# Kernel optimization log

Hardware: AMD Instinct MI355X
Metric: run time of the kernel (lower is better)

## Reference

```python
import jax, jax.numpy as jnp
import numpy as np

N_NODES = 50000
N_EDGES = 800000
NODE_DIM = 64
EDGE_DIM = 16
HIDDEN = 128
EPS = 1e-5


def _linear_init(key, fan_in, fan_out):
    k1, k2 = jax.random.split(key)
    bound = 1.0 / np.sqrt(fan_in)
    W = jax.random.uniform(k1, (fan_in, fan_out), minval=-bound, maxval=bound, dtype=jnp.float32)
    b = jax.random.uniform(k2, (fan_out,), minval=-bound, maxval=bound, dtype=jnp.float32)
    return W, b


def batchnorm(h, gamma, beta):
    # BatchNorm1d in training mode: batch mean/var (biased), eps=1e-5
    mu = jnp.mean(h, axis=0, keepdims=True)
    var = jnp.mean((h - mu) ** 2, axis=0, keepdims=True)
    return (h - mu) * jax.lax.rsqrt(var + EPS) * gamma + beta


def setup_inputs() -> dict:
    key = jax.random.key(0)
    ks = jax.random.split(key, 8)
    x = jax.random.normal(ks[0], (N_NODES, NODE_DIM), dtype=jnp.float32)
    edge_index = jax.random.randint(ks[1], (2, N_EDGES), 0, N_NODES, dtype=jnp.int64)
    edge_attr = jax.random.normal(ks[2], (N_EDGES, EDGE_DIM), dtype=jnp.float32)
    We1, be1 = _linear_init(ks[3], 2 * NODE_DIM + EDGE_DIM, HIDDEN)
    We2, be2 = _linear_init(ks[4], HIDDEN, HIDDEN)
    Wm, bm = _linear_init(ks[5], HIDDEN, HIDDEN)
    Wn1, bn1 = _linear_init(ks[6], NODE_DIM + HIDDEN, HIDDEN)
    Wn2, bn2 = _linear_init(ks[7], HIDDEN, HIDDEN)
    ones = jnp.ones((HIDDEN,), jnp.float32)
    zeros = jnp.zeros((HIDDEN,), jnp.float32)
    return dict(x=x, edge_index=edge_index, edge_attr=edge_attr,
                We1=We1, be1=be1, ge=ones, bbe=zeros, We2=We2, be2=be2,
                Wm=Wm, bm=bm,
                Wn1=Wn1, bn1=bn1, gn=ones, bbn=zeros, Wn2=Wn2, bn2=bn2)


def reference(x, edge_index, edge_attr, We1, be1, ge, bbe, We2, be2, Wm, bm, Wn1, bn1, gn, bbn, Wn2, bn2):
    row, col = edge_index[0], edge_index[1]
    # gather + concat -> edge network (Linear, BN, ReLU, Linear)
    edge_input = jnp.concatenate([x[row], x[col], edge_attr], axis=-1)  # [E, 2n+e]
    h = jax.nn.relu(batchnorm(edge_input @ We1 + be1, ge, bbe))
    edge_features = h @ We2 + be2
    # message MLP (Linear, ReLU)
    messages = jax.nn.relu(edge_features @ Wm + bm)  # [E, H]
    # scatter-add into source nodes
    agg = jax.ops.segment_sum(messages, row, num_segments=N_NODES)  # [N, H]
    # node network (Linear, BN, ReLU, Linear)
    node_input = jnp.concatenate([x, agg], axis=-1)
    hn = jax.nn.relu(batchnorm(node_input @ Wn1 + bn1, gn, bbn))
    return hn @ Wn2 + bn2
```

## Files before the change

### kernel.cpp

```cpp
#include <hip/hip_runtime.h>
#include <stdint.h>

#define NNODES 50000
#define NEDGES 800000
#define H 128
#define BN_EPS 1e-5f

typedef short short8 __attribute__((ext_vector_type(8)));
typedef float f32x4 __attribute__((ext_vector_type(4)));

__device__ __forceinline__ float bf2f(unsigned short u) {
    unsigned int v = ((unsigned int)u) << 16;
    return __uint_as_float(v);
}
__device__ __forceinline__ unsigned short f2bf(float f) {
    unsigned int x = __float_as_uint(f);
    return (unsigned short)((x + 0x7FFFu + ((x >> 16) & 1u)) >> 16);
}
__device__ __forceinline__ short8 s8z() { short8 z = {0,0,0,0,0,0,0,0}; return z; }

template<int KB>
__device__ __forceinline__ void gemm_tile(const short* __restrict__ sA, const int SK,
                                          const unsigned short* __restrict__ WT, const int RK,
                                          const int n0, f32x4 acc[4][4], const int lane) {
    const int mr = lane & 15, quad = lane >> 4;
    const short* W = (const short*)WT;
    #pragma unroll
    for (int kb = 0; kb < KB; ++kb) {
        short8 a[4];
        #pragma unroll
        for (int mt = 0; mt < 4; ++mt)
            a[mt] = *(const short8*)&sA[(mt*16 + mr)*SK + kb*32 + quad*8];
        #pragma unroll
        for (int nt = 0; nt < 4; ++nt) {
            short8 b = *(const short8*)&W[(size_t)(n0 + nt*16 + mr)*RK + kb*32 + quad*8];
            #pragma unroll
            for (int mt = 0; mt < 4; ++mt)
                acc[mt][nt] = __builtin_amdgcn_mfma_f32_16x16x32_bf16(a[mt], b, acc[mt][nt], 0, 0, 0);
        }
    }
}

__global__ void k_fold(const float* __restrict__ We2, const float* __restrict__ be2,
                       const float* __restrict__ Wm, const float* __restrict__ bm,
                       float* __restrict__ W2m, float* __restrict__ b2m) {
    int j = threadIdx.x;
    int i = blockIdx.x;
    if (i < H) {
        float acc = 0.f;
        for (int k = 0; k < H; ++k) acc = fmaf(We2[i*H + k], Wm[k*H + j], acc);
        W2m[i*H + j] = acc;
    } else {
        float acc = bm[j];
        for (int k = 0; k < H; ++k) acc = fmaf(be2[k], Wm[k*H + j], acc);
        b2m[j] = acc;
    }
}

__global__ void k_prep2(const float* __restrict__ We1, const float* __restrict__ Wn1,
                        const float* __restrict__ Wn2, const float* __restrict__ W2m,
                        unsigned short* __restrict__ WabT, unsigned short* __restrict__ Wn1T,
                        unsigned short* __restrict__ Wn2T, unsigned short* __restrict__ W2mT,
                        unsigned short* __restrict__ WcT) {
    int i = blockIdx.x*256 + threadIdx.x;
    if (i < 16384) {
        int n = i >> 6, k = i & 63;
        WabT[n*64 + k] = f2bf(We1[(n < 128 ? k : 64 + k)*H + (n & 127)]);
    } else if (i < 40960) {
        int j = i - 16384; int n = j / 192, k = j - n*192;
        Wn1T[n*192 + k] = f2bf(Wn1[k*H + n]);
    } else if (i < 57344) {
        int j = i - 40960; int n = j >> 7, k = j & 127;
        Wn2T[n*H + k] = f2bf(Wn2[k*H + n]);
    } else if (i < 73728) {
        int j = i - 57344; int n = j >> 7, k = j & 127;
        W2mT[n*H + k] = f2bf(W2m[k*H + n]);
    } else if (i < 77824) {
        int j = i - 73728; int n = j >> 5, k = j & 31;
        WcT[n*32 + k] = (k < 16) ? f2bf(We1[(128 + k)*H + n]) : (unsigned short)0;
    }
}

__global__ void k_count(const int* __restrict__ ei, int* __restrict__ cnt) {
    int e = blockIdx.x*256 + threadIdx.x;
    if (e < NEDGES) atomicAdd(&cnt[ei[e]], 1);
}

__global__ void k_scan(const int* __restrict__ cnt, int* __restrict__ offsets,
                       int* __restrict__ cursor) {
    __shared__ int wsum[16];
    __shared__ int carry;
    const int tid = threadIdx.x;
    const int lane = tid & 63, wid = tid >> 6;
    if (tid == 0) carry = 0;
    for (int base = 0; base < NNODES; base += 1024) {
        int i = base + tid;
        int v = (i < NNODES) ? cnt[i] : 0;
        int xv = v;
        #pragma unroll
        for (int off = 1; off < 64; off <<= 1) {
            int y = __shfl_up(xv, off);
            if (lane >= off) xv += y;
        }
        if (lane == 63) wsum[wid] = xv;
        __syncthreads();
        if (tid == 0) {
            int a = carry;
            #pragma unroll
            for (int j = 0; j < 16; ++j) { int t = wsum[j]; wsum[j] = a; a += t; }
            carry = a;
        }
        __syncthreads();
        int excl = wsum[wid] + xv - v;
        if (i < NNODES) { offsets[i] = excl; cursor[i] = excl; }
        __syncthreads();
    }
    if (tid == 0) offsets[NNODES] = carry;
}

__global__ void k_scatter(const int* __restrict__ ei, int* __restrict__ cursor,
                          int* __restrict__ elist) {
    int e = blockIdx.x*256 + threadIdx.x;
    if (e < NEDGES) {
        int p = atomicAdd(&cursor[ei[e]], 1);
        elist[p] = e;
    }
}

__launch_bounds__(256)
__global__ void k_T(const float* __restrict__ x, const unsigned short* __restrict__ WabT,
                    unsigned short* __restrict__ T) {
    __shared__ short sA[128*72];
    const int tid = threadIdx.x;
    const int n0b = blockIdx.x*128;
    {
        const int rowl = tid >> 1, half = (tid & 1)*32;
        const int node = n0b + rowl;
        const bool ok = node < NNODES;
        #pragma unroll
        for (int c = 0; c < 4; ++c) {
            int k0 = half + c*8;
            short8 o = s8z();
            if (ok) {
                float4 a = *(const float4*)&x[node*64 + k0];
                float4 b = *(const float4*)&x[node*64 + k0 + 4];
                o[0]=(short)f2bf(a.x); o[1]=(short)f2bf(a.y); o[2]=(short)f2bf(a.z); o[3]=(short)f2bf(a.w);
                o[4]=(short)f2bf(b.x); o[5]=(short)f2bf(b.y); o[6]=(short)f2bf(b.z); o[7]=(short)f2bf(b.w);
            }
            *(short8*)&sA[rowl*72 + k0] = o;
        }
    }
    __syncthreads();
    const int wave = tid >> 6, lane = tid & 63;
    const int m0 = (wave & 1)*64;
    const int n0 = blockIdx.y*128 + (wave >> 1)*64;
    f32x4 acc[4][4];
    f32x4 z = {0.f, 0.f, 0.f, 0.f};
    #pragma unroll
    for (int mt = 0; mt < 4; ++mt)
        #pragma unroll
        for (int nt = 0; nt < 4; ++nt) acc[mt][nt] = z;
    gemm_tile<2>(sA + m0*72, 72, WabT, 64, n0, acc, lane);
    const int mr = lane & 15, quad = lane >> 4;
    #pragma unroll
    for (int nt = 0; nt < 4; ++nt) {
        int j = n0 + nt*16 + mr;
        #pragma unroll
        for (int mt = 0; mt < 4; ++mt) {
            int nb = n0b + m0 + mt*16 + quad*4;
            #pragma unroll
            for (int r = 0; r < 4; ++r) {
                int node = nb + r;
                if (node < NNODES) T[(size_t)node*256 + j] = f2bf(acc[mt][nt][r]);
            }
        }
    }
}

__launch_bounds__(256)
__global__ void k_gather2(const unsigned short* __restrict__ T, const int* __restrict__ ei,
                          const int* __restrict__ elist, const float* __restrict__ ea,
                          const unsigned short* __restrict__ WcT, const float* __restrict__ be1,
                          unsigned short* __restrict__ hb,
                          float* __restrict__ gS, float* __restrict__ gSS) {
    __shared__ short sEa[128*40];
    __shared__ short sT[128*136];
    __shared__ float sS[H], sSS[H];
    const int tid = threadIdx.x;
    if (tid < H) { sS[tid] = 0.f; sSS[tid] = 0.f; }
    const int p0 = blockIdx.x*128;
    const int lp = tid >> 1, half = tid & 1;
    const int e = elist[p0 + lp];
    const int row = ei[e], col = ei[NEDGES + e];
    {
        const float4* ea4 = (const float4*)ea;
        float4 a = ea4[e*4 + half*2];
        float4 b = ea4[e*4 + half*2 + 1];
        short8 o;
        o[0]=(short)f2bf(a.x); o[1]=(short)f2bf(a.y); o[2]=(short)f2bf(a.z); o[3]=(short)f2bf(a.w);
        o[4]=(short)f2bf(b.x); o[5]=(short)f2bf(b.y); o[6]=(short)f2bf(b.z); o[7]=(short)f2bf(b.w);
        *(short8*)&sEa[lp*40 + half*8] = o;
        *(short8*)&sEa[lp*40 + 16 + half*8] = s8z();
    }
    {
        #pragma unroll
        for (int c = 0; c < 8; ++c) {
            int jj = half*64 + c*8;
            short8 t1 = *(const short8*)&T[(size_t)row*256 + jj];
            short8 t2 = *(const short8*)&T[(size_t)col*256 + 128 + jj];
            short8 o;
            #pragma unroll
            for (int i = 0; i < 8; ++i)
                o[i] = (short)f2bf(bf2f((unsigned short)t1[i]) + bf2f((unsigned short)t2[i]));
            *(short8*)&sT[lp*136 + jj] = o;
        }
    }
    __syncthreads();
    const int wave = tid >> 6, lane = tid & 63;
    const int m0 = (wave & 1)*64, n0 = (wave >> 1)*64;
    f32x4 acc[4][4];
    f32x4 z = {0.f, 0.f, 0.f, 0.f};
    #pragma unroll
    for (int mt = 0; mt < 4; ++mt)
        #pragma unroll
        for (int nt = 0; nt < 4; ++nt) acc[mt][nt] = z;
    gemm_tile<1>(sEa + m0*40, 40, WcT, 32, n0, acc, lane);
    const int mr = lane & 15, quad = lane >> 4;
    #pragma unroll
    for (int nt = 0; nt < 4; ++nt) {
        int j = n0 + nt*16 + mr;
        float bia = be1[j];
        float s = 0.f, ssum = 0.f;
        #pragma unroll
        for (int mt = 0; mt < 4; ++mt) {
            int m = m0 + mt*16 + quad*4;
            #pragma unroll
            for (int r = 0; r < 4; ++r) {
                float v = acc[mt][nt][r] + bf2f((unsigned short)sT[(m + r)*136 + j]) + bia;
                hb[(size_t)(p0 + m + r)*H + j] = f2bf(v);
                s += v; ssum += v*v;
            }
        }
        atomicAdd(&sS[j], s);
        atomicAdd(&sSS[j], ssum);
    }
    __syncthreads();
    if (tid < H) { atomicAdd(&gS[tid], sS[tid]); atomicAdd(&gSS[tid], sSS[tid]); }
}

__global__ void k_stats(const float* __restrict__ S, const float* __restrict__ SS,
                        const float* __restrict__ g, const float* __restrict__ b,
                        float invCount, float* __restrict__ scale, float* __restrict__ shift) {
    int j = threadIdx.x;
    float mu = S[j]*invCount;
    float var = SS[j]*invCount - mu*mu;
    float sc = rsqrtf(var + BN_EPS)*g[j];
    scale[j] = sc;
    shift[j] = b[j] - mu*sc;
}

__launch_bounds__(256)
__global__ void k_edge2(unsigned short* __restrict__ hb,
                        const float* __restrict__ scale, const float* __restrict__ shift,
                        const unsigned short* __restrict__ W2mT, const float* __restrict__ b2m) {
    __shared__ short sA[128*136];
    const int tid = threadIdx.x;
    const size_t e0 = (size_t)blockIdx.x*128;
    {
        const int rowl = tid >> 1, half = (tid & 1)*64;
        const size_t base = (e0 + rowl)*H + half;
        #pragma unroll
        for (int c = 0; c < 8; ++c) {
            int k0 = half + c*8;
            short8 raw = *(const short8*)&hb[base + c*8];
            float4 sc0 = *(const float4*)&scale[k0], sc1 = *(const float4*)&scale[k0 + 4];
            float4 sh0 = *(const float4*)&shift[k0], sh1 = *(const float4*)&shift[k0 + 4];
            short8 o;
            o[0] = (short)f2bf(fmaxf(fmaf(bf2f((unsigned short)raw[0]), sc0.x, sh0.x), 0.f));
            o[1] = (short)f2bf(fmaxf(fmaf(bf2f((unsigned short)raw[1]), sc0.y, sh0.y), 0.f));
            o[2] = (short)f2bf(fmaxf(fmaf(bf2f((unsigned short)raw[2]), sc0.z, sh0.z), 0.f));
            o[3] = (short)f2bf(fmaxf(fmaf(bf2f((unsigned short)raw[3]), sc0.w, sh0.w), 0.f));
            o[4] = (short)f2bf(fmaxf(fmaf(bf2f((unsigned short)raw[4]), sc1.x, sh1.x), 0.f));
            o[5] = (short)f2bf(fmaxf(fmaf(bf2f((unsigned short)raw[5]), sc1.y, sh1.y), 0.f));
            o[6] = (short)f2bf(fmaxf(fmaf(bf2f((unsigned short)raw[6]), sc1.z, sh1.z), 0.f));
            o[7] = (short)f2bf(fmaxf(fmaf(bf2f((unsigned short)raw[7]), sc1.w, sh1.w), 0.f));
            *(short8*)&sA[rowl*136 + k0] = o;
        }
    }
    __syncthreads();
    const int wave = tid >> 6, lane = tid & 63;
    const int m0 = (wave & 1)*64, n0 = (wave >> 1)*64;
    f32x4 acc[4][4];
    f32x4 z = {0.f, 0.f, 0.f, 0.f};
    #pragma unroll
    for (int mt = 0; mt < 4; ++mt)
        #pragma unroll
        for (int nt = 0; nt < 4; ++nt) acc[mt][nt] = z;
    gemm_tile<4>(sA + m0*136, 136, W2mT, 128, n0, acc, lane);
    const int mr = lane & 15, quad = lane >> 4;
    #pragma unroll
    for (int nt = 0; nt < 4; ++nt) {
        int j = n0 + nt*16 + mr;
        float bias = b2m[j];
        #pragma unroll
        for (int mt = 0; mt < 4; ++mt) {
            size_t eb = e0 + m0 + mt*16 + quad*4;
            #pragma unroll
            for (int r = 0; r < 4; ++r)
                hb[(eb + r)*H + j] = f2bf(fmaxf(acc[mt][nt][r] + bias, 0.f));
        }
    }
}

__launch_bounds__(256)
__global__ void k_agg(const unsigned short* __restrict__ msg, const int* __restrict__ offsets,
                      unsigned short* __restrict__ aggb) {
    const int n = blockIdx.x*4 + (threadIdx.x >> 6);
    const int lane = threadIdx.x & 63;
    const int s0 = offsets[n], t0 = offsets[n + 1];
    float a0 = 0.f, a1 = 0.f;
    for (int p = s0; p < t0; ++p) {
        unsigned int u = *(const unsigned int*)&msg[(size_t)p*H + lane*2];
        a0 += bf2f((unsigned short)(u & 0xFFFFu));
        a1 += bf2f((unsigned short)(u >> 16));
    }
    unsigned int o = (unsigned int)f2bf(a0) | ((unsigned int)f2bf(a1) << 16);
    *(unsigned int*)&aggb[(size_t)n*H + lane*2] = o;
}

__launch_bounds__(256)
__global__ void k_node1(const float* __restrict__ x, const unsigned short* __restrict__ aggb,
                        const unsigned short* __restrict__ Wn1T, const float* __restrict__ bn1,
                        float* __restrict__ h2, float* __restrict__ gS, float* __restrict__ gSS) {
    __shared__ short sA[128*200];
    __shared__ float sS[H], sSS[H];
    const int tid = threadIdx.x;
    if (tid < H) { sS[tid] = 0.f; sSS[tid] = 0.f; }
    const int n0b = blockIdx.x*128;
    {
        const int rowl = tid >> 1, half = (tid & 1)*96;
        const int node = n0b + rowl;
        const bool ok = node < NNODES;
        #pragma unroll
        for (int c = 0; c < 12; ++c) {
            int k0 = half + c*8;
            short8 o = s8z();
            if (ok) {
                if (k0 < 64) {
                    float4 a = *(const float4*)&x[node*64 + k0];
                    float4 b = *(const float4*)&x[node*64 + k0 + 4];
                    o[0]=(short)f2bf(a.x); o[1]=(short)f2bf(a.y); o[2]=(short)f2bf(a.z); o[3]=(short)f2bf(a.w);
                    o[4]=(short)f2bf(b.x); o[5]=(short)f2bf(b.y); o[6]=(short)f2bf(b.z); o[7]=(short)f2bf(b.w);
                } else {
                    o = *(const short8*)&aggb[(size_t)node*H + (k0 - 64)];
                }
            }
            *(short8*)&sA[rowl*200 + k0] = o;
        }
    }
    __syncthreads();
    const int wave = tid >> 6, lane = tid & 63;
    const int m0 = (wave & 1)*64, n0 = (wave >> 1)*64;
    f32x4 acc[4][4];
    f32x4 z = {0.f, 0.f, 0.f, 0.f};
    #pragma unroll
    for (int mt = 0; mt < 4; ++mt)
        #pragma unroll
        for (int nt = 0; nt < 4; ++nt) acc[mt][nt] = z;
    gemm_tile<6>(sA + m0*200, 200, Wn1T, 192, n0, acc, lane);
    const int mr = lane & 15, quad = lane >> 4;
    #pragma unroll
    for (int nt = 0; nt < 4; ++nt) {
        int j = n0 + nt*16 + mr;
        float bias = bn1[j];
        float s = 0.f, ssum = 0.f;
        #pragma unroll
        for (int mt = 0; mt < 4; ++mt) {
            int nb = n0b + m0 + mt*16 + quad*4;
            #pragma unroll
            for (int r = 0; r < 4; ++r) {
                int node = nb + r;
                if (node < NNODES) {
                    float v = acc[mt][nt][r] + bias;
                    h2[(size_t)node*H + j] = v;
                    s += v; ssum += v*v;
                }
            }
        }
        atomicAdd(&sS[j], s);
        atomicAdd(&sSS[j], ssum);
    }
    __syncthreads();
    if (tid < H) { atomicAdd(&gS[tid], sS[tid]); atomicAdd(&gSS[tid], sSS[tid]); }
}

__launch_bounds__(256)
__global__ void k_node2(const float* __restrict__ h2, const float* __restrict__ scale,
                        const float* __restrict__ shift, const unsigned short* __restrict__ Wn2T,
                        const float* __restrict__ bn2, float* __restrict__ out) {
    __shared__ short sA[128*136];
    const int tid = threadIdx.x;
    const int n0b = blockIdx.x*128;
    {
        const int rowl = tid >> 1, half = (tid & 1)*64;
        const int node = n0b + rowl;
        const bool ok = node < NNODES;
        #pragma unroll
        for (int c = 0; c < 8; ++c) {
            int k0 = half + c*8;
            short8 o = s8z();
            if (ok) {
                float4 a = *(const float4*)&h2[(size_t)node*H + k0];
                float4 b = *(const float4*)&h2[(size_t)node*H + k0 + 4];
                float4 sc0 = *(const float4*)&scale[k0], sc1 = *(const float4*)&scale[k0 + 4];
                float4 sh0 = *(const float4*)&shift[k0], sh1 = *(const float4*)&shift[k0 + 4];
                o[0] = (short)f2bf(fmaxf(fmaf(a.x, sc0.x, sh0.x), 0.f));
                o[1] = (short)f2bf(fmaxf(fmaf(a.y, sc0.y, sh0.y), 0.f));
                o[2] = (short)f2bf(fmaxf(fmaf(a.z, sc0.z, sh0.z), 0.f));
                o[3] = (short)f2bf(fmaxf(fmaf(a.w, sc0.w, sh0.w), 0.f));
                o[4] = (short)f2bf(fmaxf(fmaf(b.x, sc1.x, sh1.x), 0.f));
                o[5] = (short)f2bf(fmaxf(fmaf(b.y, sc1.y, sh1.y), 0.f));
                o[6] = (short)f2bf(fmaxf(fmaf(b.z, sc1.z, sh1.z), 0.f));
                o[7] = (short)f2bf(fmaxf(fmaf(b.w, sc1.w, sh1.w), 0.f));
            }
            *(short8*)&sA[rowl*136 + k0] = o;
        }
    }
    __syncthreads();
    const int wave = tid >> 6, lane = tid & 63;
    const int m0 = (wave & 1)*64, n0 = (wave >> 1)*64;
    f32x4 acc[4][4];
    f32x4 z = {0.f, 0.f, 0.f, 0.f};
    #pragma unroll
    for (int mt = 0; mt < 4; ++mt)
        #pragma unroll
        for (int nt = 0; nt < 4; ++nt) acc[mt][nt] = z;
    gemm_tile<4>(sA + m0*136, 136, Wn2T, 128, n0, acc, lane);
    const int mr = lane & 15, quad = lane >> 4;
    #pragma unroll
    for (int nt = 0; nt < 4; ++nt) {
        int j = n0 + nt*16 + mr;
        float bias = bn2[j];
        #pragma unroll
        for (int mt = 0; mt < 4; ++mt) {
            int nb = n0b + m0 + mt*16 + quad*4;
            #pragma unroll
            for (int r = 0; r < 4; ++r) {
                int node = nb + r;
                if (node < NNODES) out[(size_t)node*H + j] = acc[mt][nt][r] + bias;
            }
        }
    }
}

extern "C" void kernel_launch(void* const* d_in, const int* in_sizes, int n_in,
                              void* d_out, int out_size, void* d_ws, size_t ws_size,
                              hipStream_t stream) {
    (void)in_sizes; (void)n_in; (void)out_size; (void)ws_size;
    const float* x   = (const float*)d_in[0];
    const int*   ei  = (const int*)d_in[1];
    const float* ea  = (const float*)d_in[2];
    const float* We1 = (const float*)d_in[3];
    const float* be1 = (const float*)d_in[4];
    const float* ge  = (const float*)d_in[5];
    const float* bbe = (const float*)d_in[6];
    const float* We2 = (const float*)d_in[7];
    const float* be2 = (const float*)d_in[8];
    const float* Wm  = (const float*)d_in[9];
    const float* bm  = (const float*)d_in[10];
    const float* Wn1 = (const float*)d_in[11];
    const float* bn1 = (const float*)d_in[12];
    const float* gn  = (const float*)d_in[13];
    const float* bbn = (const float*)d_in[14];
    const float* Wn2 = (const float*)d_in[15];
    const float* bn2 = (const float*)d_in[16];
    float* out = (float*)d_out;

    char* ws = (char*)d_ws;
    unsigned short* hb   = (unsigned short*)(ws);
    unsigned short* aggb = (unsigned short*)(ws + 204800000);
    unsigned short* Tbuf = (unsigned short*)(ws + 217600000);
    float*          h2   = (float*)(ws + 217600000);
    int* cnt     = (int*)(ws + 243200000);
    int* offsets = (int*)(ws + 243400192);
    int* cursor  = (int*)(ws + 243600256);
    int* elist   = (int*)(ws + 243800320);
    float* S1     = (float*)(ws + 247000384);
    float* SS1    = S1 + 128;
    float* S2     = S1 + 256;
    float* SS2    = S1 + 384;
    float* scale1 = S1 + 512;
    float* shift1 = S1 + 640;
    float* scale2 = S1 + 768;
    float* shift2 = S1 + 896;
    float* W2m = (float*)(ws + 247004480);
    float* b2m = (float*)(ws + 247070016);
    unsigned short* WabT = (unsigned short*)(ws + 247070592);
    unsigned short* Wn1T = (unsigned short*)(ws + 247103360);
    unsigned short* Wn2T = (unsigned short*)(ws + 247152512);
    unsigned short* W2mT = (unsigned short*)(ws + 247185280);
    unsigned short* WcT  = (unsigned short*)(ws + 247218048);

    hipMemsetAsync(cnt, 0, NNODES*sizeof(int), stream);
    hipMemsetAsync(S1, 0, 512*sizeof(float), stream);

    k_fold<<<H + 1, H, 0, stream>>>(We2, be2, Wm, bm, W2m, b2m);
    k_prep2<<<304, 256, 0, stream>>>(We1, Wn1, Wn2, W2m, WabT, Wn1T, Wn2T, W2mT, WcT);
    k_count<<<NEDGES/256, 256, 0, stream>>>(ei, cnt);
    k_scan<<<1, 1024, 0, stream>>>(cnt, offsets, cursor);
    k_scatter<<<NEDGES/256, 256, 0, stream>>>(ei, cursor, elist);
    k_T<<<dim3(391, 2), 256, 0, stream>>>(x, WabT, Tbuf);
    k_gather2<<<NEDGES/128, 256, 0, stream>>>(Tbuf, ei, elist, ea, WcT, be1, hb, S1, SS1);
    k_stats<<<1, H, 0, stream>>>(S1, SS1, ge, bbe, 1.0f/NEDGES, scale1, shift1);
    k_edge2<<<NEDGES/128, 256, 0, stream>>>(hb, scale1, shift1, W2mT, b2m);
    k_agg<<<NNODES/4, 256, 0, stream>>>(hb, offsets, aggb);
    k_node1<<<391, 256, 0, stream>>>(x, aggb, Wn1T, bn1, h2, S2, SS2);
    k_stats<<<1, H, 0, stream>>>(S2, SS2, gn, bbn, 1.0f/NNODES, scale2, shift2);
    k_node2<<<391, 256, 0, stream>>>(h2, scale2, shift2, Wn2T, bn2, out);
}
```

Before: 733.3 us.

## Fuse message MLP with segmented scatter-add and stage edge-hidden stores through LDS

The second edge GEMM now reduces its output per block over runs of equal source node (edges are sorted by row), writing directly into an fp32 aggregation buffer and using atomics only for segments that cross block boundaries. This removes the separate aggregation kernel and the full write and re-read of the message tensor. The first edge kernel also stages its hidden output in shared memory and writes it out as coalesced 16-byte rows instead of scattered 2-byte stores. In exchange it adds a memset of the aggregation buffer, fp32 atomics, and a serial per-thread segment scan over 128 rows.

```diff
diff --git a/kernel.cpp b/kernel.cpp
--- a/kernel.cpp
+++ b/kernel.cpp
@@ -237,7 +237,7 @@
             #pragma unroll
             for (int r = 0; r < 4; ++r) {
                 float v = acc[mt][nt][r] + bf2f((unsigned short)sT[(m + r)*136 + j]) + bia;
-                hb[(size_t)(p0 + m + r)*H + j] = f2bf(v);
+                sT[(m + r)*136 + j] = (short)f2bf(v);
                 s += v; ssum += v*v;
             }
         }
@@ -245,6 +245,12 @@
         atomicAdd(&sSS[j], ssum);
     }
     __syncthreads();
+    {
+        const int hh = half*64;
+        #pragma unroll
+        for (int c = 0; c < 8; ++c)
+            *(short8*)&hb[(size_t)(p0 + lp)*H + hh + c*8] = *(const short8*)&sT[lp*136 + hh + c*8];
+    }
     if (tid < H) { atomicAdd(&gS[tid], sS[tid]); atomicAdd(&gSS[tid], sSS[tid]); }
 }
 
@@ -260,15 +266,19 @@
 }
 
 __launch_bounds__(256)
-__global__ void k_edge2(unsigned short* __restrict__ hb,
-                        const float* __restrict__ scale, const float* __restrict__ shift,
-                        const unsigned short* __restrict__ W2mT, const float* __restrict__ b2m) {
+__global__ void k_fused2(const unsigned short* __restrict__ hb,
+                         const float* __restrict__ scale, const float* __restrict__ shift,
+                         const unsigned short* __restrict__ W2mT, const float* __restrict__ b2m,
+                         const int* __restrict__ ei, const int* __restrict__ elist,
+                         const int* __restrict__ offsets, float* __restrict__ agg) {
     __shared__ short sA[128*136];
+    __shared__ int rows[128];
     const int tid = threadIdx.x;
-    const size_t e0 = (size_t)blockIdx.x*128;
+    const int p0 = blockIdx.x*128;
+    if (tid < 128) rows[tid] = ei[elist[p0 + tid]];
     {
         const int rowl = tid >> 1, half = (tid & 1)*64;
-        const size_t base = (e0 + rowl)*H + half;
+        const size_t base = ((size_t)p0 + rowl)*H + half;
         #pragma unroll
         for (int c = 0; c < 8; ++c) {
             int k0 = half + c*8;
@@ -297,6 +307,7 @@
         #pragma unroll
         for (int nt = 0; nt < 4; ++nt) acc[mt][nt] = z;
     gemm_tile<4>(sA + m0*136, 136, W2mT, 128, n0, acc, lane);
+    __syncthreads();
     const int mr = lane & 15, quad = lane >> 4;
     #pragma unroll
     for (int nt = 0; nt < 4; ++nt) {
@@ -304,32 +315,33 @@
         float bias = b2m[j];
         #pragma unroll
         for (int mt = 0; mt < 4; ++mt) {
-            size_t eb = e0 + m0 + mt*16 + quad*4;
+            int m = m0 + mt*16 + quad*4;
             #pragma unroll
             for (int r = 0; r < 4; ++r)
-                hb[(eb + r)*H + j] = f2bf(fmaxf(acc[mt][nt][r] + bias, 0.f));
+                sA[(m + r)*136 + j] = (short)f2bf(fmaxf(acc[mt][nt][r] + bias, 0.f));
+        }
+    }
+    __syncthreads();
+    if (tid < 128) {
+        const int jf = tid;
+        int p = 0;
+        while (p < 128) {
+            int r = rows[p];
+            int q = p + 1;
+            while (q < 128 && rows[q] == r) ++q;
+            float sum = 0.f;
+            for (int i = p; i < q; ++i) sum += bf2f((unsigned short)sA[i*136 + jf]);
+            bool full = (p0 + p == offsets[r]) && (p0 + q == offsets[r + 1]);
+            float* dst = &agg[(size_t)r*H + jf];
+            if (full) *dst = sum;
+            else atomicAdd(dst, sum);
+            p = q;
         }
     }
 }
 
 __launch_bounds__(256)
-__global__ void k_agg(const unsigned short* __restrict__ msg, const int* __restrict__ offsets,
-                      unsigned short* __restrict__ aggb) {
-    const int n = blockIdx.x*4 + (threadIdx.x >> 6);
-    const int lane = threadIdx.x & 63;
-    const int s0 = offsets[n], t0 = offsets[n + 1];
-    float a0 = 0.f, a1 = 0.f;
-    for (int p = s0; p < t0; ++p) {
-        unsigned int u = *(const unsigned int*)&msg[(size_t)p*H + lane*2];
-        a0 += bf2f((unsigned short)(u & 0xFFFFu));
-        a1 += bf2f((unsigned short)(u >> 16));
-    }
-    unsigned int o = (unsigned int)f2bf(a0) | ((unsigned int)f2bf(a1) << 16);
-    *(unsigned int*)&aggb[(size_t)n*H + lane*2] = o;
-}
-
-__launch_bounds__(256)
-__global__ void k_node1(const float* __restrict__ x, const unsigned short* __restrict__ aggb,
+__global__ void k_node1(const float* __restrict__ x, const float* __restrict__ agg,
                         const unsigned short* __restrict__ Wn1T, const float* __restrict__ bn1,
                         float* __restrict__ h2, float* __restrict__ gS, float* __restrict__ gSS) {
     __shared__ short sA[128*200];
@@ -346,14 +358,16 @@
             int k0 = half + c*8;
             short8 o = s8z();
             if (ok) {
+                float4 a, b;
                 if (k0 < 64) {
-                    float4 a = *(const float4*)&x[node*64 + k0];
-                    float4 b = *(const float4*)&x[node*64 + k0 + 4];
-                    o[0]=(short)f2bf(a.x); o[1]=(short)f2bf(a.y); o[2]=(short)f2bf(a.z); o[3]=(short)f2bf(a.w);
-                    o[4]=(short)f2bf(b.x); o[5]=(short)f2bf(b.y); o[6]=(short)f2bf(b.z); o[7]=(short)f2bf(b.w);
+                    a = *(const float4*)&x[node*64 + k0];
+                    b = *(const float4*)&x[node*64 + k0 + 4];
                 } else {
-                    o = *(const short8*)&aggb[(size_t)node*H + (k0 - 64)];
+                    a = *(const float4*)&agg[(size_t)node*H + (k0 - 64)];
+                    b = *(const float4*)&agg[(size_t)node*H + (k0 - 64) + 4];
                 }
+                o[0]=(short)f2bf(a.x); o[1]=(short)f2bf(a.y); o[2]=(short)f2bf(a.z); o[3]=(short)f2bf(a.w);
+                o[4]=(short)f2bf(b.x); o[5]=(short)f2bf(b.y); o[6]=(short)f2bf(b.z); o[7]=(short)f2bf(b.w);
             }
             *(short8*)&sA[rowl*200 + k0] = o;
         }
@@ -478,14 +492,14 @@
 
     char* ws = (char*)d_ws;
     unsigned short* hb   = (unsigned short*)(ws);
-    unsigned short* aggb = (unsigned short*)(ws + 204800000);
-    unsigned short* Tbuf = (unsigned short*)(ws + 217600000);
-    float*          h2   = (float*)(ws + 217600000);
-    int* cnt     = (int*)(ws + 243200000);
-    int* offsets = (int*)(ws + 243400192);
-    int* cursor  = (int*)(ws + 243600256);
-    int* elist   = (int*)(ws + 243800320);
-    float* S1     = (float*)(ws + 247000384);
+    float*          h2   = (float*)(ws + 204800000);
+    int* cnt     = (int*)(ws + 204800000);
+    int* offsets = (int*)(ws + 205000192);
+    int* cursor  = (int*)(ws + 205200256);
+    int* elist   = (int*)(ws + 205400320);
+    unsigned short* Tbuf = (unsigned short*)(ws + 230400000);
+    float*          agg  = (float*)(ws + 230400000);
+    float* S1     = (float*)(ws + 256000000);
     float* SS1    = S1 + 128;
     float* S2     = S1 + 256;
     float* SS2    = S1 + 384;
@@ -493,13 +507,13 @@
     float* shift1 = S1 + 640;
     float* scale2 = S1 + 768;
     float* shift2 = S1 + 896;
-    float* W2m = (float*)(ws + 247004480);
-    float* b2m = (float*)(ws + 247070016);
-    unsigned short* WabT = (unsigned short*)(ws + 247070592);
-    unsigned short* Wn1T = (unsigned short*)(ws + 247103360);
-    unsigned short* Wn2T = (unsigned short*)(ws + 247152512);
-    unsigned short* W2mT = (unsigned short*)(ws + 247185280);
-    unsigned short* WcT  = (unsigned short*)(ws + 247218048);
+    float* W2m = (float*)(ws + 256004096);
+    float* b2m = (float*)(ws + 256069632);
+    unsigned short* WabT = (unsigned short*)(ws + 256070144);
+    unsigned short* Wn1T = (unsigned short*)(ws + 256102912);
+    unsigned short* Wn2T = (unsigned short*)(ws + 256152064);
+    unsigned short* W2mT = (unsigned short*)(ws + 256184832);
+    unsigned short* WcT  = (unsigned short*)(ws + 256217600);
 
     hipMemsetAsync(cnt, 0, NNODES*sizeof(int), stream);
     hipMemsetAsync(S1, 0, 512*sizeof(float), stream);
@@ -512,9 +526,10 @@
     k_T<<<dim3(391, 2), 256, 0, stream>>>(x, WabT, Tbuf);
     k_gather2<<<NEDGES/128, 256, 0, stream>>>(Tbuf, ei, elist, ea, WcT, be1, hb, S1, SS1);
     k_stats<<<1, H, 0, stream>>>(S1, SS1, ge, bbe, 1.0f/NEDGES, scale1, shift1);
-    k_edge2<<<NEDGES/128, 256, 0, stream>>>(hb, scale1, shift1, W2mT, b2m);
-    k_agg<<<NNODES/4, 256, 0, stream>>>(hb, offsets, aggb);
-    k_node1<<<391, 256, 0, stream>>>(x, aggb, Wn1T, bn1, h2, S2, SS2);
+    hipMemsetAsync(agg, 0, (size_t)NNODES*H*sizeof(float), stream);
+    k_fused2<<<NEDGES/128, 256, 0, stream>>>(hb, scale1, shift1, W2mT, b2m,
+                                             ei, elist, offsets, agg);
+    k_node1<<<391, 256, 0, stream>>>(x, agg, Wn1T, bn1, h2, S2, SS2);
     k_stats<<<1, H, 0, stream>>>(S2, SS2, gn, bbn, 1.0f/NNODES, scale2, shift2);
     k_node2<<<391, 256, 0, stream>>>(h2, scale2, shift2, Wn2T, bn2, out);
 }
```

Result: slower. 754.8 us (+2.9%).
